# Performance work log

Hardware: AMD Instinct MI355X
Metric: run time of the kernel (lower is better)

Reference implementation:

```python
import jax, jax.numpy as jnp
from jax import lax
import numpy as np

# Module config (from init_kwargs)
NUM_SEG_ROW = 8
NUM_SEG_COL = 8
H = 224
W = 224
K = NUM_SEG_ROW * NUM_SEG_COL  # 64 labels
B = 4


def setup_inputs() -> dict:
    key = jax.random.key(0)
    grad_map = jax.random.normal(key, (B, 1, H, W), dtype=jnp.float32)
    return {"grad_map": grad_map, "band_width": 5, "num_iterations": 5}


def _dp_paths(neg_g):
    """Dynamic-programming min-cost path. neg_g: (L, P, M) per-step costs.
    Returns positions (L, P): index in [0, M) chosen at each step."""
    L, P, M = neg_g.shape
    m = jnp.arange(M)
    # clamp(m + {-1,0,1}, 0, M-1); torch's inf padding is never hit after clamping
    nbr = jnp.clip(m[:, None] + jnp.array([-1, 0, 1])[None, :], 0, M - 1)  # (M,3)

    def step(prev_cost, g_row):
        pc = prev_cost[:, nbr]                      # (P, M, 3)
        amin = pc.argmin(axis=2)                    # (P, M)
        min_prev = jnp.take_along_axis(pc, amin[..., None], axis=2)[..., 0]
        path_row = nbr[m[None, :], amin]            # (P, M) predecessor position
        new_cost = min_prev + g_row
        return new_cost, (new_cost, path_row)

    _, (costs, paths) = lax.scan(step, neg_g[0], neg_g[1:])  # paths: (L-1, P, M)
    idx_last = costs[-1].argmin(axis=1)             # (P,)

    def back(idx, path_row):
        new_idx = path_row[jnp.arange(path_row.shape[0]), idx]
        return new_idx, idx

    first_idx, pos_tail = lax.scan(back, idx_last, paths, reverse=True)
    positions = jnp.concatenate([first_idx[None], pos_tail], axis=0)  # (L, P)
    return positions


def _boundary_masks(grad2d, x_inits, y_inits, band_width):
    """grad2d: (H, W). Returns (vmask, hmask) boolean (H, W)."""
    offs = jnp.arange(-band_width, band_width + 1)
    P = x_inits.shape[0]
    # vertical paths (one x per row)
    x_idx = jnp.clip(x_inits[:, None] + offs[None, :], 0, W - 1)   # (P, M)
    pos_v = _dp_paths(-grad2d[:, x_idx])                            # (H, P)
    coords_v = x_idx[jnp.arange(P)[None, :], pos_v]                 # (H, P) x-coords
    vmask = jnp.zeros((H, W), bool).at[jnp.arange(H)[:, None], coords_v].set(True)
    # horizontal paths (one y per column)
    y_idx = jnp.clip(y_inits[:, None] + offs[None, :], 0, H - 1)    # (P, M)
    pos_h = _dp_paths(-grad2d.T[:, y_idx])                          # (W, P)
    coords_h = y_idx[jnp.arange(P)[None, :], pos_h]                 # (W, P) y-coords
    hmask = jnp.zeros((H, W), bool).at[coords_h, jnp.arange(W)[:, None]].set(True)
    return vmask, hmask


def _one_hot_nchw(labels):
    return jax.nn.one_hot(labels, K, dtype=jnp.float32).transpose(0, 3, 1, 2)


def _box_vote(oh, ksize):
    # grouped (depthwise) conv with all-ones kernel == neighborhood vote count
    kern = jnp.ones((K, 1, ksize, ksize), oh.dtype)
    pad = ksize // 2
    return lax.conv_general_dilated(
        oh, kern, window_strides=(1, 1), padding=[(pad, pad), (pad, pad)],
        dimension_numbers=("NCHW", "OIHW", "NCHW"), feature_group_count=K)


def reference(grad_map, band_width, num_iterations):
    x_inits = jnp.clip(jnp.array([i * (W // NUM_SEG_COL) for i in range(1, NUM_SEG_COL)]), 0, W - 1)
    y_inits = jnp.clip(jnp.array([i * (H // NUM_SEG_ROW) for i in range(1, NUM_SEG_ROW)]), 0, H - 1)
    vmask, hmask = jax.vmap(lambda g: _boundary_masks(g, x_inits, y_inits, band_width))(grad_map[:, 0])
    v_labels = jnp.cumsum(vmask.astype(jnp.int32), axis=2)
    h_labels = jnp.cumsum(hmask.astype(jnp.int32), axis=1)
    seg = v_labels + NUM_SEG_COL * h_labels                         # (B, H, W), values in [0, K)
    # multi-scale connectivity voting
    oh = _one_hot_nchw(seg)
    labels = seg
    for _ in range(num_iterations):
        vote_sum = _box_vote(oh, 3) + _box_vote(oh, 5) + _box_vote(oh, 7)
        labels = vote_sum.argmax(axis=1)
        oh = _one_hot_nchw(labels)
    return labels
```

## Files before the change

kernel.cpp:

```cpp
#include <hip/hip_runtime.h>
#include <stdint.h>

#define HH 224
#define WW 224
#define BB 4
#define PP 7
#define SEG 28
#define BW 5
#define MM 11

#define POS_INF_I 0x7F800000

typedef const __attribute__((address_space(1))) unsigned int* gas_ptr;
typedef __attribute__((address_space(3))) unsigned int* las_ptr;
typedef unsigned long long ull;

__device__ inline ull mcompose(ull F, ull G) {
    ull H = 0ull;
#pragma unroll
    for (int i = 0; i < 11; ++i) {
        unsigned g = (unsigned)(G >> (4 * i)) & 15u;
        H |= ((F >> (4 * g)) & 15ull) << (4 * i);
    }
    return H;
}

__global__ __launch_bounds__(64) void dp_kernel(const float* __restrict__ grad,
                                                int* __restrict__ coords_v,
                                                int* __restrict__ coords_h) {
    __shared__ __align__(16) float gseg[225 * 16];

    const int tid = threadIdx.x;
    const int l   = tid & 15;
    const int sid = blockIdx.x;
    const int p   = sid % PP;
    const int dir = (sid / PP) & 1;
    const int b   = sid / (2 * PP);
    const int base = SEG * (p + 1);
    const float* gb = grad + b * (HH * WW);

    {
        const int r  = tid >> 4;
        const int m  = tid & 15;
        const int sS = (dir == 0) ? WW : 1;
        const int sM = (dir == 0) ? 1  : WW;
        const float* src = gb + r * sS + (base - BW + m) * sM;
        const long stepBytes = (long)(4 * sS) * 4;
#pragma unroll 8
        for (int c = 0; c < 56; ++c) {
            __builtin_amdgcn_global_load_lds((gas_ptr)(const void*)src,
                                             (las_ptr)(void*)(&gseg[c * 64]), 4, 0, 0);
            src = (const float*)((const char*)src + stepBytes);
        }
    }
    __syncthreads();

    const float lane_add = (l < MM) ? 0.0f : __int_as_float(POS_INF_I);
    const float* gp = &gseg[l];

    unsigned wreg[16] = {};

#define DP_STEP(gval, ownb, jj_c)                                                       \
    {                                                                                   \
        float v1 = cost;                                                                \
        float v0 = __int_as_float(__builtin_amdgcn_update_dpp(                          \
            POS_INF_I, __float_as_int(cost), 0x111, 0xf, 0xf, false));                  \
        float v2 = __int_as_float(__builtin_amdgcn_update_dpp(                          \
            POS_INF_I, __float_as_int(cost), 0x101, 0xf, 0xf, false));                  \
        bool a01 = (v0 <= v1), a02 = (v0 <= v2), a12 = (v1 <= v2);                      \
        bool aa  = a01 && a02;                                                          \
        unsigned long long A   = __ballot(aa);                                          \
        unsigned long long C12 = __ballot(a12);                                         \
        unsigned long long B0 = ~A & C12;                                               \
        unsigned long long B1 = ~A & ~C12;                                              \
        float mv = aa ? v0 : (a12 ? v1 : v2);                                           \
        cost = mv - (gval) + lane_add;                                                  \
        unsigned wv = (unsigned)(B0 & 0x7FFull) | ((unsigned)(B1 & 0x7FFull) << 11);    \
        wreg[(jj_c)] = (ownb) ? wv : wreg[(jj_c)];                                      \
    }

    float cost = -gp[0] + lane_add;
    float buf[16], c0[16];
#pragma unroll
    for (int k = 0; k < 16; ++k) buf[k] = gp[(1 + k) * 16];
    for (int t = 0; t < 13; ++t) {
        const bool own = (tid == t);
#pragma unroll
        for (int k = 0; k < 16; ++k) c0[k] = buf[k];
#pragma unroll
        for (int k = 0; k < 16; ++k) buf[k] = gp[(16 * (t + 1) + 1 + k) * 16];
#pragma unroll
        for (int k = 0; k < 16; ++k) DP_STEP(c0[k], own, k)
    }
    {
        const bool own = (tid == 13);
#pragma unroll
        for (int k = 0; k < 15; ++k) DP_STEP(buf[k], own, k)
    }
#undef DP_STEP

    float bc = cost;
    int   bi = l;
#pragma unroll
    for (int mask = 1; mask < 16; mask <<= 1) {
        float oc = __shfl_xor(bc, mask, 16);
        int   oi = __shfl_xor(bi, mask, 16);
        if (oc < bc || (oc == bc && oi < bi)) { bc = oc; bi = oi; }
    }
    const int idx_last = bi;

    const int mcnt = (l < 13) ? 16 : ((l == 13) ? 15 : 0);
    const ull IDMAP = 0xA9876543210ull;
    ull L = IDMAP;
#pragma unroll
    for (int jj = 15; jj >= 0; --jj) {
        if (jj < mcnt) {
            unsigned ww = wreg[jj];
            ull M = 0ull;
#pragma unroll
            for (int i = 0; i < MM; ++i) {
                unsigned sel = ((ww >> i) & 1u) + 2u * ((ww >> (11 + i)) & 1u);
                M |= ((ull)(i + (int)sel - 1)) << (4 * i);
            }
            L = mcompose(M, L);
        }
    }
    ull I = L;
#pragma unroll
    for (int d = 1; d < 16; d <<= 1) {
        ull O = __shfl_down(I, d, 16);
        if (l + d < 16) I = mcompose(I, O);
    }
    ull R = __shfl_down(I, 1, 16);
    if (l == 15) R = IDMAP;

    int* cout = (dir == 0) ? coords_v : coords_h;
    if (tid == 15) cout[(b * HH + 223) * PP + p] = base + idx_last - BW;
    if (tid < 16) {
        unsigned v = (unsigned)(R >> (4 * idx_last)) & 15u;
#pragma unroll
        for (int jj = 15; jj >= 0; --jj) {
            if (jj < mcnt) {
                unsigned ww = wreg[jj];
                unsigned sel = ((ww >> v) & 1u) + 2u * ((ww >> (11 + v)) & 1u);
                v = v + sel - 1u;
                cout[(b * HH + (16 * l + jj)) * PP + p] = base + (int)v - BW;
            }
        }
    }
}

#define RW 38
#define RH 14
#define RSTR 40

__device__ __forceinline__ int slow_vote_bins(const ull* rows, int x, int y, int t,
                                              unsigned* __restrict__ bins) {
#pragma unroll
    for (int c = 0; c < 16; ++c) bins[c * 256 + t] = 0u;
#pragma unroll
    for (int dy = -3; dy <= 3; ++dy) {
        if ((unsigned)(y + dy) >= (unsigned)HH) continue;
        ull row = rows[dy + 3];
        const int ay = dy < 0 ? -dy : dy;
#pragma unroll
        for (int dx = -3; dx <= 3; ++dx) {
            if ((unsigned)(x + dx) >= (unsigned)WW) continue;
            int lb = (int)((row >> (8 * (dx + 3))) & 255u);
            const int ax = dx < 0 ? -dx : dx;
            const int d = ay > ax ? ay : ax;
            const unsigned wgt = (d <= 1) ? 3u : (unsigned)(4 - d);
            atomicAdd(&bins[(lb >> 2) * 256 + t], wgt << ((lb & 3) * 8));
        }
    }
    int best_s = 0, best_k = 0;
#pragma unroll
    for (int c = 0; c < 16; ++c) {
        unsigned wd = bins[c * 256 + t];
        if (wd) {
#pragma unroll
            for (int q = 0; q < 4; ++q) {
                int s = (int)((wd >> (q * 8)) & 255u);
                if (s > best_s) { best_s = s; best_k = c * 4 + q; }
            }
        }
    }
    return best_k;
}

#define SW_K1   0x0001010101010101ull
#define SW_HI7  0x0080808080808080ull
#define SW_LO7  0x007F7F7F7F7F7F7Full
#define SW_W1   0x0001020303030201ull
#define SW_W2   0x0001020202020201ull

__device__ __forceinline__ ull sw_zm(ull xv) {
    return (~(((xv & SW_LO7) + SW_LO7) | xv)) & SW_HI7;
}
__device__ __forceinline__ int sw_dotm(ull m, ull W) {
    return (int)((((m >> 7) * W) >> 48) & 0xFFull);
}

__device__ __forceinline__ int swar_or_bins(const ull* rows, int x, int y,
                                            unsigned cl, int t,
                                            unsigned* __restrict__ bins) {
    ull vmx = SW_HI7;
    if (x < 3)   vmx &= (~0ull) << (8 * (3 - x));
    if (x > 220) vmx &= (1ull << (8 * (227 - x))) - 1ull;

    unsigned c1 = 254u, c2 = 254u, c3 = 254u;
    int s0 = 0, s1 = 0, s2 = 0, s3 = 0;
    bool ovf = false;
    const ull rep0 = (ull)cl * SW_K1;

#pragma unroll
    for (int r = 0; r < 7; ++r) {
        if ((unsigned)(y + r - 3) >= (unsigned)HH) continue;
        const ull row = rows[r];
        const int ay   = r < 3 ? 3 - r : r - 3;
        const bool POPC = (ay == 3);
        const ull W    = (ay <= 1) ? SW_W1 : SW_W2;

        ull e0 = sw_zm(row ^ rep0) & vmx;
        ull e1 = sw_zm(row ^ ((ull)c1 * SW_K1)) & vmx;
        ull e2 = sw_zm(row ^ ((ull)c2 * SW_K1)) & vmx;
        ull e3 = sw_zm(row ^ ((ull)c3 * SW_K1)) & vmx;
        s0 += POPC ? __popcll(e0) : sw_dotm(e0, W);
        s1 += POPC ? __popcll(e1) : sw_dotm(e1, W);
        s2 += POPC ? __popcll(e2) : sw_dotm(e2, W);
        s3 += POPC ? __popcll(e3) : sw_dotm(e3, W);

        ull rem = vmx & ~(e0 | e1 | e2 | e3);
        for (int it = 0; it < 3 && rem; ++it) {
            int pos = (int)__builtin_ctzll(rem);
            unsigned nb = (unsigned)((row >> (pos - 7)) & 255u);
            ull en = sw_zm(row ^ ((ull)nb * SW_K1)) & vmx;
            int dn = POPC ? __popcll(en) : sw_dotm(en, W);
            if      (c1 == 254u) { c1 = nb; s1 += dn; }
            else if (c2 == 254u) { c2 = nb; s2 += dn; }
            else if (c3 == 254u) { c3 = nb; s3 += dn; }
            else ovf = true;
            rem &= ~en;
        }
        if (rem) ovf = true;
    }

    if (ovf) return slow_vote_bins(rows, x, y, t, bins);

    int bs = s0; unsigned bl = cl;
    if (s1 > bs || (s1 == bs && c1 < bl)) { bs = s1; bl = c1; }
    if (s2 > bs || (s2 == bs && c2 < bl)) { bs = s2; bl = c2; }
    if (s3 > bs || (s3 == bs && c3 < bl)) { bs = s3; bl = c3; }
    return (int)bl;
}

__device__ __forceinline__ void gather_rows_lds(const unsigned char* lab,
                                                int tx, int ty, ull* rows) {
#pragma unroll
    for (int r = 0; r < 7; ++r) {
        int o  = (ty + r) * RSTR + tx;
        int a8 = o & ~7;
        int sh = (o & 7) * 8;
        ull lo = *reinterpret_cast<const ull*>(lab + a8);
        ull hi = *reinterpret_cast<const ull*>(lab + a8 + 8);
        ull row = lo >> sh;
        if (sh) row |= hi << (64 - sh);
        rows[r] = row & 0x00FFFFFFFFFFFFFFull;
    }
}

__global__ __launch_bounds__(256) void labvote_kernel(const int* __restrict__ cv,
                                                      const int* __restrict__ ch,
                                                      unsigned char* __restrict__ out8) {
    __shared__ __align__(8) unsigned char lab[RH * RSTR];
    __shared__ unsigned bins[16 * 256];
    const int tx = threadIdx.x, ty = threadIdx.y;
    const int t  = ty * 32 + tx;
    const int b  = blockIdx.z;
    const int GX0 = blockIdx.x * 32, GY0 = blockIdx.y * 8;

    for (int idx = t; idx < RW * RH; idx += 256) {
        int j = idx / RW, i = idx - j * RW;
        int gxc = min(max(GX0 - 3 + i, 0), WW - 1);
        int gyc = min(max(GY0 - 3 + j, 0), HH - 1);
        const int* cvp = cv + (b * HH + gyc) * PP;
        const int* chp = ch + (b * WW + gxc) * PP;
        int v = 0, h = 0;
#pragma unroll
        for (int q = 0; q < PP; ++q) { v += (cvp[q] <= gxc); h += (chp[q] <= gyc); }
        lab[j * RSTR + i] = (unsigned char)(v + 8 * h);
    }
    __syncthreads();

    const int x = GX0 + tx, y = GY0 + ty;
    ull rows[7];
    gather_rows_lds(lab, tx, ty, rows);

    const unsigned labc = (unsigned)((rows[3] >> 24) & 255u);
    const ull rep = (ull)labc * SW_K1;
    bool uni = true;
#pragma unroll
    for (int k = 0; k < 7; ++k) uni = uni && (rows[k] == rep);

    int best_k = uni ? (int)labc : swar_or_bins(rows, x, y, labc, t, bins);
    out8[(b * HH + y) * WW + x] = (unsigned char)best_k;
}

__global__ __launch_bounds__(256) void vote_kernel(const unsigned char* __restrict__ in,
                                                   unsigned char* __restrict__ out8,
                                                   int* __restrict__ out32) {
    __shared__ __align__(8) unsigned char lab[RH * RSTR];
    __shared__ unsigned bins[16 * 256];
    __shared__ int blkuni;
    const int tx = threadIdx.x, ty = threadIdx.y;
    const int t  = ty * 32 + tx;
    const int x  = blockIdx.x * 32 + tx;
    const int y  = blockIdx.y * 8 + ty;
    const int b  = blockIdx.z;
    const int GX0 = blockIdx.x * 32, GY0 = blockIdx.y * 8;
    const unsigned char* img = in + b * (HH * WW);

    if (t == 0) blkuni = 1;
    for (int idx = t; idx < RW * RH; idx += 256) {
        int j = idx / RW, i = idx - j * RW;
        int gxc = min(max(GX0 - 3 + i, 0), WW - 1);
        int gyc = min(max(GY0 - 3 + j, 0), HH - 1);
        lab[j * RSTR + i] = img[gyc * WW + gxc];
    }
    __syncthreads();

    {
        const unsigned char ref = lab[0];
        int ok = 1;
        for (int idx = t; idx < RW * RH; idx += 256) {
            int j = idx / RW, i = idx - j * RW;
            ok &= (lab[j * RSTR + i] == ref);
        }
        if (!ok) blkuni = 0;
        __syncthreads();
        if (blkuni) {
            int o = (b * HH + y) * WW + x;
            if (out8)  out8[o]  = ref;
            if (out32) out32[o] = (int)ref;
            return;
        }
    }

    ull rows[7];
    gather_rows_lds(lab, tx, ty, rows);

    const unsigned labc = (unsigned)((rows[3] >> 24) & 255u);
    const ull rep = (ull)labc * SW_K1;
    bool uni = true;
#pragma unroll
    for (int k = 0; k < 7; ++k) uni = uni && (rows[k] == rep);

    int best_k = uni ? (int)labc : swar_or_bins(rows, x, y, labc, t, bins);

    int o = (b * HH + y) * WW + x;
    if (out8)  out8[o]  = (unsigned char)best_k;
    if (out32) out32[o] = best_k;
}

extern "C" void kernel_launch(void* const* d_in, const int* in_sizes, int n_in,
                              void* d_out, int out_size, void* d_ws, size_t ws_size,
                              hipStream_t stream) {
    (void)in_sizes; (void)n_in; (void)out_size; (void)ws_size;
    const float* grad = (const float*)d_in[0];
    int* out = (int*)d_out;
    char* ws = (char*)d_ws;

    int* cv = (int*)(ws);
    int* ch = (int*)(ws + 25088);
    unsigned char* laW = (unsigned char*)(ws + 50176);
    unsigned char* laD = (unsigned char*)d_out;

    dp_kernel<<<56, 64, 0, stream>>>(grad, cv, ch);

    dim3 grid(WW / 32, HH / 8, BB), blk(32, 8, 1);
    labvote_kernel<<<grid, blk, 0, stream>>>(cv, ch, laD);
    vote_kernel<<<grid, blk, 0, stream>>>(laD, laW, nullptr);
    vote_kernel<<<grid, blk, 0, stream>>>(laW, laD, nullptr);
    vote_kernel<<<grid, blk, 0, stream>>>(laD, laW, nullptr);
    vote_kernel<<<grid, blk, 0, stream>>>(laW, nullptr, out);
}
```

Measured before the change: 123.5 us.

## Fuse vote iterations into two kernels using halo recomputation in shared memory

Replaces the label kernel plus four separate vote kernels with two kernels. The first builds labels and runs two vote iterations, and the second runs three vote iterations, each computing enlarged halo tiles in LDS so that several iterations run without a global round-trip or an extra launch. This removes three kernel launches and their intermediate global traffic. In exchange it adds redundant halo computation and more LDS, and drops the whole-block uniform early exit.

```diff
diff --git a/kernel.cpp b/kernel.cpp
--- a/kernel.cpp
+++ b/kernel.cpp
@@ -14,6 +14,10 @@
 typedef const __attribute__((address_space(1))) unsigned int* gas_ptr;
 typedef __attribute__((address_space(3))) unsigned int* las_ptr;
 typedef unsigned long long ull;
+
+__device__ __forceinline__ int iclamp(int v, int lo, int hi) {
+    return min(max(v, lo), hi);
+}
 
 __device__ inline ull mcompose(ull F, ull G) {
     ull H = 0ull;
@@ -150,10 +154,6 @@
     }
 }
 
-#define RW 38
-#define RH 14
-#define RSTR 40
-
 __device__ __forceinline__ int slow_vote_bins(const ull* rows, int x, int y, int t,
                                               unsigned* __restrict__ bins) {
 #pragma unroll
@@ -254,11 +254,12 @@
     return (int)bl;
 }
 
-__device__ __forceinline__ void gather_rows_lds(const unsigned char* lab,
-                                                int tx, int ty, ull* rows) {
+template<int STR>
+__device__ __forceinline__ void gather7(const unsigned char* lab,
+                                        int cx0, int cy0, ull* rows) {
 #pragma unroll
     for (int r = 0; r < 7; ++r) {
-        int o  = (ty + r) * RSTR + tx;
+        int o  = (cy0 + r) * STR + cx0;
         int a8 = o & ~7;
         int sh = (o & 7) * 8;
         ull lo = *reinterpret_cast<const ull*>(lab + a8);
@@ -269,97 +270,126 @@
     }
 }
 
-__global__ __launch_bounds__(256) void labvote_kernel(const int* __restrict__ cv,
-                                                      const int* __restrict__ ch,
-                                                      unsigned char* __restrict__ out8) {
-    __shared__ __align__(8) unsigned char lab[RH * RSTR];
+__device__ __forceinline__ int do_vote(const ull* rows, int x, int y, int t,
+                                       unsigned* __restrict__ bins) {
+    const unsigned cl = (unsigned)((rows[3] >> 24) & 255u);
+    const ull rep = (ull)cl * SW_K1;
+    bool uni = true;
+#pragma unroll
+    for (int k = 0; k < 7; ++k) uni = uni && (rows[k] == rep);
+    if (uni) return (int)cl;
+    return swar_or_bins(rows, x, y, cl, t, bins);
+}
+
+__global__ __launch_bounds__(256) void labvote2_kernel(const int* __restrict__ cv,
+                                                       const int* __restrict__ ch,
+                                                       unsigned char* __restrict__ out8) {
+    __shared__ int cvs[20 * PP];
+    __shared__ int chs[44 * PP];
+    __shared__ __align__(8) unsigned char labR[20 * 48];
+    __shared__ __align__(8) unsigned char labS[14 * 40];
     __shared__ unsigned bins[16 * 256];
+
     const int tx = threadIdx.x, ty = threadIdx.y;
     const int t  = ty * 32 + tx;
     const int b  = blockIdx.z;
     const int GX0 = blockIdx.x * 32, GY0 = blockIdx.y * 8;
 
-    for (int idx = t; idx < RW * RH; idx += 256) {
-        int j = idx / RW, i = idx - j * RW;
-        int gxc = min(max(GX0 - 3 + i, 0), WW - 1);
-        int gyc = min(max(GY0 - 3 + j, 0), HH - 1);
-        const int* cvp = cv + (b * HH + gyc) * PP;
-        const int* chp = ch + (b * WW + gxc) * PP;
+    for (int idx = t; idx < 20 * PP; idx += 256) {
+        int gyc = iclamp(GY0 - 6 + idx / PP, 0, HH - 1);
+        cvs[idx] = cv[(b * HH + gyc) * PP + idx % PP];
+    }
+    for (int idx = t; idx < 44 * PP; idx += 256) {
+        int gxc = iclamp(GX0 - 6 + idx / PP, 0, WW - 1);
+        chs[idx] = ch[(b * WW + gxc) * PP + idx % PP];
+    }
+    __syncthreads();
+
+    for (int idx = t; idx < 44 * 20; idx += 256) {
+        int j = idx / 44, i = idx - j * 44;
+        int gxc = iclamp(GX0 - 6 + i, 0, WW - 1);
+        int gyc = iclamp(GY0 - 6 + j, 0, HH - 1);
         int v = 0, h = 0;
 #pragma unroll
-        for (int q = 0; q < PP; ++q) { v += (cvp[q] <= gxc); h += (chp[q] <= gyc); }
-        lab[j * RSTR + i] = (unsigned char)(v + 8 * h);
-    }
-    __syncthreads();
-
-    const int x = GX0 + tx, y = GY0 + ty;
-    ull rows[7];
-    gather_rows_lds(lab, tx, ty, rows);
-
-    const unsigned labc = (unsigned)((rows[3] >> 24) & 255u);
-    const ull rep = (ull)labc * SW_K1;
-    bool uni = true;
-#pragma unroll
-    for (int k = 0; k < 7; ++k) uni = uni && (rows[k] == rep);
-
-    int best_k = uni ? (int)labc : swar_or_bins(rows, x, y, labc, t, bins);
-    out8[(b * HH + y) * WW + x] = (unsigned char)best_k;
-}
-
-__global__ __launch_bounds__(256) void vote_kernel(const unsigned char* __restrict__ in,
-                                                   unsigned char* __restrict__ out8,
-                                                   int* __restrict__ out32) {
-    __shared__ __align__(8) unsigned char lab[RH * RSTR];
+        for (int q = 0; q < PP; ++q) {
+            v += (cvs[j * PP + q] <= gxc);
+            h += (chs[i * PP + q] <= gyc);
+        }
+        labR[j * 48 + i] = (unsigned char)(v + 8 * h);
+    }
+    __syncthreads();
+
+    for (int idx = t; idx < 38 * 14; idx += 256) {
+        int j = idx / 38, i = idx - j * 38;
+        int gxc = iclamp(GX0 - 3 + i, 0, WW - 1);
+        int gyc = iclamp(GY0 - 3 + j, 0, HH - 1);
+        int cx0 = gxc - GX0 + 3;
+        int cy0 = gyc - GY0 + 3;
+        ull rows[7];
+        gather7<48>(labR, cx0, cy0, rows);
+        labS[j * 40 + i] = (unsigned char)do_vote(rows, gxc, gyc, t, bins);
+    }
+    __syncthreads();
+
+    {
+        const int x = GX0 + tx, y = GY0 + ty;
+        ull rows[7];
+        gather7<40>(labS, tx, ty, rows);
+        out8[(b * HH + y) * WW + x] = (unsigned char)do_vote(rows, x, y, t, bins);
+    }
+}
+
+__global__ __launch_bounds__(256) void vote3_kernel(const unsigned char* __restrict__ in,
+                                                    int* __restrict__ out32) {
+    __shared__ __align__(8) unsigned char labA[26 * 56];
+    __shared__ __align__(8) unsigned char labB[20 * 48];
+    __shared__ __align__(8) unsigned char labC[14 * 40];
     __shared__ unsigned bins[16 * 256];
-    __shared__ int blkuni;
+
     const int tx = threadIdx.x, ty = threadIdx.y;
     const int t  = ty * 32 + tx;
-    const int x  = blockIdx.x * 32 + tx;
-    const int y  = blockIdx.y * 8 + ty;
     const int b  = blockIdx.z;
     const int GX0 = blockIdx.x * 32, GY0 = blockIdx.y * 8;
     const unsigned char* img = in + b * (HH * WW);
 
-    if (t == 0) blkuni = 1;
-    for (int idx = t; idx < RW * RH; idx += 256) {
-        int j = idx / RW, i = idx - j * RW;
-        int gxc = min(max(GX0 - 3 + i, 0), WW - 1);
-        int gyc = min(max(GY0 - 3 + j, 0), HH - 1);
-        lab[j * RSTR + i] = img[gyc * WW + gxc];
+    for (int idx = t; idx < 50 * 26; idx += 256) {
+        int j = idx / 50, i = idx - j * 50;
+        int gxc = iclamp(GX0 - 9 + i, 0, WW - 1);
+        int gyc = iclamp(GY0 - 9 + j, 0, HH - 1);
+        labA[j * 56 + i] = img[gyc * WW + gxc];
+    }
+    __syncthreads();
+
+    for (int idx = t; idx < 44 * 20; idx += 256) {
+        int j = idx / 44, i = idx - j * 44;
+        int gxc = iclamp(GX0 - 6 + i, 0, WW - 1);
+        int gyc = iclamp(GY0 - 6 + j, 0, HH - 1);
+        int cx0 = gxc - GX0 + 6;
+        int cy0 = gyc - GY0 + 6;
+        ull rows[7];
+        gather7<56>(labA, cx0, cy0, rows);
+        labB[j * 48 + i] = (unsigned char)do_vote(rows, gxc, gyc, t, bins);
+    }
+    __syncthreads();
+
+    for (int idx = t; idx < 38 * 14; idx += 256) {
+        int j = idx / 38, i = idx - j * 38;
+        int gxc = iclamp(GX0 - 3 + i, 0, WW - 1);
+        int gyc = iclamp(GY0 - 3 + j, 0, HH - 1);
+        int cx0 = gxc - GX0 + 3;
+        int cy0 = gyc - GY0 + 3;
+        ull rows[7];
+        gather7<48>(labB, cx0, cy0, rows);
+        labC[j * 40 + i] = (unsigned char)do_vote(rows, gxc, gyc, t, bins);
     }
     __syncthreads();
 
     {
-        const unsigned char ref = lab[0];
-        int ok = 1;
-        for (int idx = t; idx < RW * RH; idx += 256) {
-            int j = idx / RW, i = idx - j * RW;
-            ok &= (lab[j * RSTR + i] == ref);
-        }
-        if (!ok) blkuni = 0;
-        __syncthreads();
-        if (blkuni) {
-            int o = (b * HH + y) * WW + x;
-            if (out8)  out8[o]  = ref;
-            if (out32) out32[o] = (int)ref;
-            return;
-        }
-    }
-
-    ull rows[7];
-    gather_rows_lds(lab, tx, ty, rows);
-
-    const unsigned labc = (unsigned)((rows[3] >> 24) & 255u);
-    const ull rep = (ull)labc * SW_K1;
-    bool uni = true;
-#pragma unroll
-    for (int k = 0; k < 7; ++k) uni = uni && (rows[k] == rep);
-
-    int best_k = uni ? (int)labc : swar_or_bins(rows, x, y, labc, t, bins);
-
-    int o = (b * HH + y) * WW + x;
-    if (out8)  out8[o]  = (unsigned char)best_k;
-    if (out32) out32[o] = best_k;
+        const int x = GX0 + tx, y = GY0 + ty;
+        ull rows[7];
+        gather7<40>(labC, tx, ty, rows);
+        out32[(b * HH + y) * WW + x] = do_vote(rows, x, y, t, bins);
+    }
 }
 
 extern "C" void kernel_launch(void* const* d_in, const int* in_sizes, int n_in,
@@ -373,14 +403,10 @@
     int* cv = (int*)(ws);
     int* ch = (int*)(ws + 25088);
     unsigned char* laW = (unsigned char*)(ws + 50176);
-    unsigned char* laD = (unsigned char*)d_out;
 
     dp_kernel<<<56, 64, 0, stream>>>(grad, cv, ch);
 
     dim3 grid(WW / 32, HH / 8, BB), blk(32, 8, 1);
-    labvote_kernel<<<grid, blk, 0, stream>>>(cv, ch, laD);
-    vote_kernel<<<grid, blk, 0, stream>>>(laD, laW, nullptr);
-    vote_kernel<<<grid, blk, 0, stream>>>(laW, laD, nullptr);
-    vote_kernel<<<grid, blk, 0, stream>>>(laD, laW, nullptr);
-    vote_kernel<<<grid, blk, 0, stream>>>(laW, nullptr, out);
-}
+    labvote2_kernel<<<grid, blk, 0, stream>>>(cv, ch, laW);
+    vote3_kernel<<<grid, blk, 0, stream>>>(laW, out);
+}
```

Result: slower. 148.4 us (+20.1%).
